# Kernel tuning notes

Hardware: AMD Instinct MI355X
Metric: run time of the kernel (lower is better)

The kernel has to match this reference:

```python
import jax, jax.numpy as jnp
import numpy as np

NUM_HEADS = 16
EMBED_DIM = 1024
HEAD_DIM = EMBED_DIM // NUM_HEADS


def setup_inputs() -> dict:
    key = jax.random.key(0)
    ks = jax.random.split(key, 9)
    B, S, D = 4, 2048, EMBED_DIM
    scale = 1.0 / np.sqrt(D)
    inp = {
        "x": jax.random.normal(ks[0], (B, S, D), dtype=jnp.float32),
        "Wq": jax.random.normal(ks[1], (D, D), dtype=jnp.float32) * scale,
        "bq": jnp.zeros((D,), dtype=jnp.float32),
        "Wk": jax.random.normal(ks[2], (D, D), dtype=jnp.float32) * scale,
        "bk": jnp.zeros((D,), dtype=jnp.float32),
        "Wv": jax.random.normal(ks[3], (D, D), dtype=jnp.float32) * scale,
        "bv": jnp.zeros((D,), dtype=jnp.float32),
        "Wo": jax.random.normal(ks[4], (D, D), dtype=jnp.float32) * scale,
        "bo": jnp.zeros((D,), dtype=jnp.float32),
    }
    return inp


def reference(x, Wq, bq, Wk, bk, Wv, bv, Wo, bo):
    # x: [B, S, D]; weights stored torch-style as [out, in] -> use x @ W.T + b
    B, S, D = x.shape
    H, Hd = NUM_HEADS, HEAD_DIM

    def proj(W, b):
        return (jnp.einsum('bsd,ed->bse', x, W) + b).reshape(B, S, H, Hd).transpose(0, 2, 1, 3)

    Q = proj(Wq, bq)  # [B, H, S, Hd]
    K = proj(Wk, bk)
    V = proj(Wv, bv)

    scores = jnp.einsum('bhqd,bhkd->bhqk', Q, K) / jnp.sqrt(jnp.float32(Hd))
    attn = jax.nn.softmax(scores, axis=-1)  # dropout is identity in eval mode
    context = jnp.einsum('bhqk,bhkd->bhqd', attn, V)
    context = context.transpose(0, 2, 1, 3).reshape(B, S, D)
    out = jnp.einsum('bsd,ed->bse', context, Wo) + bo
    return out
```

## Files before the change

### kernel.cpp

```cpp
#include <hip/hip_runtime.h>


#define LOG2E 1.4426950408889634f
#define QSCALE (0.125f * LOG2E)

typedef __bf16 bf16x8 __attribute__((ext_vector_type(8)));
typedef float f32x4 __attribute__((ext_vector_type(4)));
typedef float f32x2 __attribute__((ext_vector_type(2)));
typedef unsigned short u16x4 __attribute__((ext_vector_type(4)));
typedef unsigned short u16x8 __attribute__((ext_vector_type(8)));
typedef unsigned int u32x4 __attribute__((ext_vector_type(4)));

__device__ __forceinline__ unsigned short f2bf(float f) {
  unsigned int u = __builtin_bit_cast(unsigned int, f);
  u += 0x7fffu + ((u >> 16) & 1u);
  return (unsigned short)(u >> 16);
}

__device__ __forceinline__ unsigned int cvtpk(float a, float b) {
  unsigned int r;
  asm("v_cvt_pk_bf16_f32 %0, %1, %2" : "=v"(r) : "v"(a), "v"(b));
  return r;
}

typedef const __attribute__((address_space(1))) void* gptr_t;
typedef __attribute__((address_space(3))) void* lptr_t;
__device__ __forceinline__ void gload16(const void* g, void* l) {
  __builtin_amdgcn_global_load_lds((gptr_t)g, (lptr_t)l, 16, 0, 0);
}

__global__ __launch_bounds__(256) void k_cvt(const float* __restrict__ x,
                                             const float* __restrict__ Wq, const float* __restrict__ Wk,
                                             const float* __restrict__ Wv, const float* __restrict__ Wo,
                                             unsigned short* __restrict__ xb, unsigned short* __restrict__ Wb) {
  int gi = (blockIdx.x * 256 + threadIdx.x) * 4;
  if (gi < 8388608) {
    f32x4 v = *(const f32x4*)(x + gi);
    u16x4 o; o[0] = f2bf(v[0]); o[1] = f2bf(v[1]); o[2] = f2bf(v[2]); o[3] = f2bf(v[3]);
    *(u16x4*)(xb + gi) = o;
  } else {
    int i = gi - 8388608;
    int wsel = i >> 20;
    int loc = i & 1048575;
    const float* src = (wsel == 0) ? Wq : (wsel == 1) ? Wk : (wsel == 2) ? Wv : Wo;
    float sc = (wsel == 0) ? QSCALE : 1.0f;
    f32x4 v = *(const f32x4*)(src + loc);
    u16x4 o; o[0] = f2bf(v[0] * sc); o[1] = f2bf(v[1] * sc); o[2] = f2bf(v[2] * sc); o[3] = f2bf(v[3] * sc);
    *(u16x4*)(Wb + i) = o;
  }
}

__global__ __launch_bounds__(256, 3) void k_gemm_qkv(
    const unsigned short* __restrict__ xb, const unsigned short* __restrict__ Wb,
    const float* __restrict__ bq, const float* __restrict__ bk, const float* __restrict__ bv,
    unsigned short* __restrict__ Qb, unsigned short* __restrict__ Kb, unsigned short* __restrict__ Vtb) {
  __shared__ unsigned short As[2 * 4096];
  __shared__ unsigned short Bs[2 * 4096];
  const int tid = threadIdx.x;
  const int lane = tid & 63;
  const int w = tid >> 6;
  const int wm = w & 1;
  const int wn = w >> 1;
  const int lin = blockIdx.x + (blockIdx.y << 3) + (blockIdx.z << 9);
  const int swz = (lin & 7) * 192 + (lin >> 3);
  const int z = swz >> 9;
  const int m0 = ((swz >> 3) & 63) << 7;
  const int n0 = (swz & 7) << 7;
  const unsigned short* W = Wb + ((size_t)z << 20);

  const int sR = tid >> 3;
  const int sc_ = (tid & 7) ^ (sR & 7);
  const int mrow0 = 2 * sR + (sc_ >> 2);
  const int kc0 = (sc_ & 3) << 3;
  const unsigned short* srcA = xb + (size_t)(m0 + mrow0) * 1024 + kc0;
  const unsigned short* srcB = W + (size_t)(n0 + mrow0) * 1024 + kc0;
  unsigned short* dstA = As + tid * 8;
  unsigned short* dstB = Bs + tid * 8;

  const int fr = lane & 15;
  const int kq = lane >> 4;
  int aoff[4], boff[4];
#pragma unroll
  for (int t = 0; t < 4; ++t) {
    int ra = wm * 64 + t * 16 + fr;
    aoff[t] = ((ra >> 1) << 6) + (((((ra & 1) << 2) + kq) ^ ((ra >> 1) & 7)) << 3);
    int rb = wn * 64 + t * 16 + fr;
    boff[t] = ((rb >> 1) << 6) + (((((rb & 1) << 2) + kq) ^ ((rb >> 1) & 7)) << 3);
  }

  f32x4 zero4 = {0.f, 0.f, 0.f, 0.f};
  f32x4 acc[4][4];
#pragma unroll
  for (int i = 0; i < 4; ++i)
#pragma unroll
    for (int jj = 0; jj < 4; ++jj) acc[i][jj] = zero4;

  gload16(srcA, dstA);
  gload16(srcA + 65536, dstA + 2048);
  gload16(srcB, dstB);
  gload16(srcB + 65536, dstB + 2048);

  int cur = 0;
  for (int kt = 0; kt < 32; ++kt) {
    const int kon = ((kt + 1) & 31) << 5;
    const int soff = (cur ^ 1) << 12;
    gload16(srcA + kon, dstA + soff);
    gload16(srcA + 65536 + kon, dstA + soff + 2048);
    gload16(srcB + kon, dstB + soff);
    gload16(srcB + 65536 + kon, dstB + soff + 2048);

    asm volatile("s_waitcnt vmcnt(4)" ::: "memory");
    __builtin_amdgcn_s_barrier();

    const unsigned short* Ac = As + (cur << 12);
    const unsigned short* Bc = Bs + (cur << 12);
    bf16x8 af[4], bfr[4];
#pragma unroll
    for (int mt = 0; mt < 4; ++mt) af[mt] = *(const bf16x8*)&Ac[aoff[mt]];
#pragma unroll
    for (int nt = 0; nt < 4; ++nt) bfr[nt] = *(const bf16x8*)&Bc[boff[nt]];

    asm volatile("s_waitcnt lgkmcnt(0)" ::: "memory");
    __builtin_amdgcn_s_barrier();

    __builtin_amdgcn_s_setprio(1);
#pragma unroll
    for (int mt = 0; mt < 4; ++mt)
#pragma unroll
      for (int nt = 0; nt < 4; ++nt)
        acc[mt][nt] = __builtin_amdgcn_mfma_f32_16x16x32_bf16(af[mt], bfr[nt], acc[mt][nt], 0, 0, 0);
    __builtin_amdgcn_s_setprio(0);
    cur ^= 1;
  }

  const float* bias = (z == 0) ? bq : (z == 1) ? bk : bv;
  const float bsc = (z == 0) ? QSCALE : 1.0f;
  const int rg = kq << 2;
#pragma unroll
  for (int mt = 0; mt < 4; ++mt) {
    const int mb = m0 + wm * 64 + mt * 16 + rg;
    const int b = mb >> 11;
    const int s = mb & 2047;
#pragma unroll
    for (int nt = 0; nt < 4; ++nt) {
      const int n = n0 + wn * 64 + nt * 16 + fr;
      const float bvv = bias[n] * bsc;
      const int h = n >> 6;
      const int d = n & 63;
      if (z == 2) {
        u16x4 pk;
#pragma unroll
        for (int r = 0; r < 4; ++r) pk[r] = f2bf(acc[mt][nt][r] + bvv);
        const int pbase = (s & ~31) | ((s & 12) << 1) | ((s & 16) >> 2);
        *(u16x4*)&Vtb[(((size_t)(b * 16 + h) << 6) + d) * 2048 + pbase] = pk;
      } else {
        unsigned short* O = (z == 0) ? Qb : Kb;
#pragma unroll
        for (int r = 0; r < 4; ++r)
          O[(((size_t)(b * 16 + h) << 11) + s + r) * 64 + d] = f2bf(acc[mt][nt][r] + bvv);
      }
    }
  }
}

__global__ __launch_bounds__(512, 4) void k_flash(
    const unsigned short* __restrict__ Qb, const unsigned short* __restrict__ Kb,
    const unsigned short* __restrict__ Vtb, unsigned short* __restrict__ Ctx) {
  __shared__ unsigned short Ks[2 * 128 * 64];
  __shared__ unsigned short Vts[64 * 128];
  const int tid = threadIdx.x;
  const int lane = tid & 63;
  const int wq = tid >> 6;
  const int fr = lane & 15;
  const int qd = lane >> 4;
  const int lin = blockIdx.x + (blockIdx.y << 3);
  const int swz = ((lin & 7) << 6) + (lin >> 3);
  const int bh = swz >> 3;
  const int q0 = (swz & 7) << 8;
  const size_t hoff = (size_t)bh << 17;
  const unsigned short* Qh = Qb + hoff + ((size_t)q0 << 6);

  const unsigned short* kg[2];
  const unsigned short* vg[2];
  unsigned short* kl[2];
  unsigned short* vl[2];
#pragma unroll
  for (int p = 0; p < 2; ++p) {
    int slot = p * 512 + tid;
    int kr = slot >> 3, ch = slot & 7;
    kg[p] = Kb + hoff + (size_t)kr * 64 + ((ch ^ (kr & 7)) << 3);
    kl[p] = Ks + slot * 8;
    int dr = slot >> 4, ch2 = slot & 15;
    vg[p] = Vtb + hoff + (size_t)dr * 2048 + ((ch2 ^ (dr & 15)) << 3);
    vl[p] = Vts + slot * 8;
  }

  int kbase[2];
#pragma unroll
  for (int ds = 0; ds < 2; ++ds)
    kbase[ds] = fr * 64 + (((ds * 4 + qd) ^ (fr & 7)) << 3);
  int vbase[4];
#pragma unroll
  for (int ks = 0; ks < 4; ++ks)
    vbase[ks] = fr * 128 + (((ks * 4 + qd) ^ fr) << 3);

  bf16x8 qf[2][2];
#pragma unroll
  for (int qt = 0; qt < 2; ++qt)
#pragma unroll
    for (int ds = 0; ds < 2; ++ds)
      qf[qt][ds] = *(const bf16x8*)&Qh[(wq * 32 + qt * 16 + fr) * 64 + ds * 32 + qd * 8];

  f32x4 zero4 = {0.f, 0.f, 0.f, 0.f};
  f32x4 o_acc[2][4];
  f32x2 l2[2] = {{0.f, 0.f}, {0.f, 0.f}};
#pragma unroll
  for (int mt = 0; mt < 2; ++mt)
#pragma unroll
    for (int dt = 0; dt < 4; ++dt) o_acc[mt][dt] = zero4;

#pragma unroll
  for (int p = 0; p < 2; ++p) gload16(kg[p], kl[p]);
#pragma unroll
  for (int p = 0; p < 2; ++p) kg[p] += 128 * 64;
  __syncthreads();

  int curoff = 0;
  for (int j = 0; j < 16; ++j) {
#pragma unroll
    for (int p = 0; p < 2; ++p) gload16(vg[p], vl[p]);
#pragma unroll
    for (int p = 0; p < 2; ++p) gload16(kg[p], kl[p] + (curoff ^ 8192));
#pragma unroll
    for (int p = 0; p < 2; ++p) { kg[p] += 128 * 64; vg[p] += 128; }

    const unsigned short* Kc = Ks + curoff;
    u32x4 pfw[2][4];
#pragma unroll
    for (int ks = 0; ks < 4; ++ks) {
      f32x4 st0[2], st1[2];
      st0[0] = zero4; st0[1] = zero4; st1[0] = zero4; st1[1] = zero4;
      __builtin_amdgcn_s_setprio(1);
#pragma unroll
      for (int ds = 0; ds < 2; ++ds) {
        bf16x8 kf0 = *(const bf16x8*)&Kc[kbase[ds] + (2 * ks) * 1024];
        bf16x8 kf1 = *(const bf16x8*)&Kc[kbase[ds] + (2 * ks + 1) * 1024];
        st0[0] = __builtin_amdgcn_mfma_f32_16x16x32_bf16(kf0, qf[0][ds], st0[0], 0, 0, 0);
        st0[1] = __builtin_amdgcn_mfma_f32_16x16x32_bf16(kf0, qf[1][ds], st0[1], 0, 0, 0);
        st1[0] = __builtin_amdgcn_mfma_f32_16x16x32_bf16(kf1, qf[0][ds], st1[0], 0, 0, 0);
        st1[1] = __builtin_amdgcn_mfma_f32_16x16x32_bf16(kf1, qf[1][ds], st1[1], 0, 0, 0);
      }
      __builtin_amdgcn_s_setprio(0);
#pragma unroll
      for (int mt = 0; mt < 2; ++mt) {
#pragma unroll
        for (int r = 0; r < 4; ++r) {
          st0[mt][r] = __builtin_amdgcn_exp2f(st0[mt][r]);
          st1[mt][r] = __builtin_amdgcn_exp2f(st1[mt][r]);
        }
        f32x2 s01 = {st0[mt][0], st0[mt][1]};
        f32x2 s23 = {st0[mt][2], st0[mt][3]};
        f32x2 t01 = {st1[mt][0], st1[mt][1]};
        f32x2 t23 = {st1[mt][2], st1[mt][3]};
        l2[mt] += (s01 + s23) + (t01 + t23);
        u32x4 pk;
        pk[0] = cvtpk(st0[mt][0], st0[mt][1]);
        pk[1] = cvtpk(st0[mt][2], st0[mt][3]);
        pk[2] = cvtpk(st1[mt][0], st1[mt][1]);
        pk[3] = cvtpk(st1[mt][2], st1[mt][3]);
        pfw[mt][ks] = pk;
      }
    }

    asm volatile("s_waitcnt vmcnt(2)" ::: "memory");
    __builtin_amdgcn_s_barrier();

    __builtin_amdgcn_s_setprio(1);
#pragma unroll
    for (int ks = 0; ks < 4; ++ks) {
      bf16x8 pf0 = __builtin_bit_cast(bf16x8, pfw[0][ks]);
      bf16x8 pf1 = __builtin_bit_cast(bf16x8, pfw[1][ks]);
#pragma unroll
      for (int dt = 0; dt < 4; ++dt) {
        bf16x8 vf = *(const bf16x8*)&Vts[vbase[ks] + dt * 2048];
        o_acc[0][dt] = __builtin_amdgcn_mfma_f32_16x16x32_bf16(pf0, vf, o_acc[0][dt], 0, 0, 0);
        o_acc[1][dt] = __builtin_amdgcn_mfma_f32_16x16x32_bf16(pf1, vf, o_acc[1][dt], 0, 0, 0);
      }
    }
    __builtin_amdgcn_s_setprio(0);

    asm volatile("s_waitcnt vmcnt(0)" ::: "memory");
    __builtin_amdgcn_s_barrier();
    curoff ^= 8192;
  }

  float l_red[2];
#pragma unroll
  for (int mt = 0; mt < 2; ++mt) {
    float lv = l2[mt][0] + l2[mt][1];
    lv += __shfl_xor(lv, 16);
    lv += __shfl_xor(lv, 32);
    l_red[mt] = lv;
  }

  const int b = bh >> 4;
  const int h = bh & 15;
#pragma unroll
  for (int mt = 0; mt < 2; ++mt) {
#pragma unroll
    for (int r = 0; r < 4; ++r) {
      float lv = __shfl(l_red[mt], qd * 4 + r);
      float rl = 1.0f / lv;
      int s = q0 + wq * 32 + mt * 16 + qd * 4 + r;
      size_t base = (((size_t)b * 2048 + s) << 10) + (h << 6);
#pragma unroll
      for (int dt = 0; dt < 4; ++dt) Ctx[base + dt * 16 + fr] = f2bf(o_acc[mt][dt][r] * rl);
    }
  }
}

__global__ __launch_bounds__(256, 3) void k_gemm_out(
    const unsigned short* __restrict__ Ctx, const unsigned short* __restrict__ Wo,
    const float* __restrict__ bo, float* __restrict__ out) {
  __shared__ unsigned short As[2 * 4096];
  __shared__ unsigned short Bs[2 * 4096];
  const int tid = threadIdx.x;
  const int lane = tid & 63;
  const int w = tid >> 6;
  const int wm = w & 1;
  const int wn = w >> 1;
  const int lin = blockIdx.x + (blockIdx.y << 3);
  const int swz = ((lin & 7) << 6) + (lin >> 3);
  const int m0 = (swz >> 3) << 7;
  const int n0 = (swz & 7) << 7;

  const int sR = tid >> 3;
  const int sc_ = (tid & 7) ^ (sR & 7);
  const int mrow0 = 2 * sR + (sc_ >> 2);
  const int kc0 = (sc_ & 3) << 3;
  const unsigned short* srcA = Ctx + (size_t)(m0 + mrow0) * 1024 + kc0;
  const unsigned short* srcB = Wo + (size_t)(n0 + mrow0) * 1024 + kc0;
  unsigned short* dstA = As + tid * 8;
  unsigned short* dstB = Bs + tid * 8;

  const int fr = lane & 15;
  const int kq = lane >> 4;
  int aoff[4], boff[4];
#pragma unroll
  for (int t = 0; t < 4; ++t) {
    int ra = wm * 64 + t * 16 + fr;
    aoff[t] = ((ra >> 1) << 6) + (((((ra & 1) << 2) + kq) ^ ((ra >> 1) & 7)) << 3);
    int rb = wn * 64 + t * 16 + fr;
    boff[t] = ((rb >> 1) << 6) + (((((rb & 1) << 2) + kq) ^ ((rb >> 1) & 7)) << 3);
  }

  f32x4 zero4 = {0.f, 0.f, 0.f, 0.f};
  f32x4 acc[4][4];
#pragma unroll
  for (int i = 0; i < 4; ++i)
#pragma unroll
    for (int jj = 0; jj < 4; ++jj) acc[i][jj] = zero4;

  gload16(srcA, dstA);
  gload16(srcA + 65536, dstA + 2048);
  gload16(srcB, dstB);
  gload16(srcB + 65536, dstB + 2048);

  int cur = 0;
  for (int kt = 0; kt < 32; ++kt) {
    const int kon = ((kt + 1) & 31) << 5;
    const int soff = (cur ^ 1) << 12;
    gload16(srcA + kon, dstA + soff);
    gload16(srcA + 65536 + kon, dstA + soff + 2048);
    gload16(srcB + kon, dstB + soff);
    gload16(srcB + 65536 + kon, dstB + soff + 2048);

    asm volatile("s_waitcnt vmcnt(4)" ::: "memory");
    __builtin_amdgcn_s_barrier();

    const unsigned short* Ac = As + (cur << 12);
    const unsigned short* Bc = Bs + (cur << 12);
    bf16x8 af[4], bfr[4];
#pragma unroll
    for (int mt = 0; mt < 4; ++mt) af[mt] = *(const bf16x8*)&Ac[aoff[mt]];
#pragma unroll
    for (int nt = 0; nt < 4; ++nt) bfr[nt] = *(const bf16x8*)&Bc[boff[nt]];

    asm volatile("s_waitcnt lgkmcnt(0)" ::: "memory");
    __builtin_amdgcn_s_barrier();

    __builtin_amdgcn_s_setprio(1);
#pragma unroll
    for (int mt = 0; mt < 4; ++mt)
#pragma unroll
      for (int nt = 0; nt < 4; ++nt)
        acc[mt][nt] = __builtin_amdgcn_mfma_f32_16x16x32_bf16(af[mt], bfr[nt], acc[mt][nt], 0, 0, 0);
    __builtin_amdgcn_s_setprio(0);
    cur ^= 1;
  }

  const int rg = kq << 2;
#pragma unroll
  for (int mt = 0; mt < 4; ++mt) {
    const int mb = m0 + wm * 64 + mt * 16 + rg;
#pragma unroll
    for (int nt = 0; nt < 4; ++nt) {
      const int n = n0 + wn * 64 + nt * 16 + fr;
      const float bvv = bo[n];
#pragma unroll
      for (int r = 0; r < 4; ++r)
        out[(size_t)(mb + r) * 1024 + n] = acc[mt][nt][r] + bvv;
    }
  }
}

extern "C" void kernel_launch(void* const* d_in, const int* in_sizes, int n_in,
                              void* d_out, int out_size, void* d_ws, size_t ws_size,
                              hipStream_t stream) {
  (void)in_sizes; (void)n_in; (void)out_size; (void)ws_size;
  const float* x = (const float*)d_in[0];
  const float* Wq = (const float*)d_in[1];
  const float* bq = (const float*)d_in[2];
  const float* Wk = (const float*)d_in[3];
  const float* bk = (const float*)d_in[4];
  const float* Wv = (const float*)d_in[5];
  const float* bv = (const float*)d_in[6];
  const float* Wo = (const float*)d_in[7];
  const float* bo = (const float*)d_in[8];
  float* out = (float*)d_out;

  unsigned short* xb = (unsigned short*)d_ws;
  unsigned short* Wb = xb + 8388608;
  unsigned short* Qb = Wb + 4194304;
  unsigned short* Kb = Qb + 8388608;
  unsigned short* Vtb = Kb + 8388608;
  unsigned short* Ctx = xb;

  k_cvt<<<12288, 256, 0, stream>>>(x, Wq, Wk, Wv, Wo, xb, Wb);
  k_gemm_qkv<<<dim3(8, 64, 3), 256, 0, stream>>>(xb, Wb, bq, bk, bv, Qb, Kb, Vtb);
  k_flash<<<dim3(8, 64), 512, 0, stream>>>(Qb, Kb, Vtb, Ctx);
  k_gemm_out<<<dim3(8, 64), 256, 0, stream>>>(Ctx, Wb + 3 * 1048576, bo, out);
}
```

Before: 263.0 us.

## Enlarge QKV GEMM tiles to 256x256 with 512 threads and deeper K steps

Rewrites the QKV projection GEMM to use 256x256 output tiles per block with 8 waves, a K step of 64, and a new LDS layout with XOR swizzle. Inside each K step it double-buffers the A fragment reads from shared memory so they overlap the MFMAs. The grid becomes 384 blocks with a new swizzle mapping. The aim is to raise arithmetic intensity and cut global and LDS traffic per FLOP, at the cost of 128 KB of LDS, more registers per thread, and fewer blocks (384 over 256 CUs), which risks poor occupancy and tail imbalance.

```diff
diff --git a/kernel.cpp b/kernel.cpp
--- a/kernel.cpp
+++ b/kernel.cpp
@@ -50,95 +50,116 @@
   }
 }
 
-__global__ __launch_bounds__(256, 3) void k_gemm_qkv(
+__global__ __launch_bounds__(512, 2) void k_gemm_qkv(
     const unsigned short* __restrict__ xb, const unsigned short* __restrict__ Wb,
     const float* __restrict__ bq, const float* __restrict__ bk, const float* __restrict__ bv,
     unsigned short* __restrict__ Qb, unsigned short* __restrict__ Kb, unsigned short* __restrict__ Vtb) {
-  __shared__ unsigned short As[2 * 4096];
-  __shared__ unsigned short Bs[2 * 4096];
+  __shared__ unsigned short As[2 * 16384];
+  __shared__ unsigned short Bs[2 * 16384];
   const int tid = threadIdx.x;
   const int lane = tid & 63;
   const int w = tid >> 6;
-  const int wm = w & 1;
-  const int wn = w >> 1;
-  const int lin = blockIdx.x + (blockIdx.y << 3) + (blockIdx.z << 9);
-  const int swz = (lin & 7) * 192 + (lin >> 3);
-  const int z = swz >> 9;
-  const int m0 = ((swz >> 3) & 63) << 7;
-  const int n0 = (swz & 7) << 7;
+  const int wm = w >> 2;
+  const int wn = w & 3;
+  const int lin = blockIdx.x;
+  const int swz = (lin & 7) * 48 + (lin >> 3);
+  const int z = swz >> 7;
+  const int t7 = swz & 127;
+  const int m0 = (t7 >> 2) << 8;
+  const int n0 = (t7 & 3) << 8;
   const unsigned short* W = Wb + ((size_t)z << 20);
 
-  const int sR = tid >> 3;
-  const int sc_ = (tid & 7) ^ (sR & 7);
-  const int mrow0 = 2 * sR + (sc_ >> 2);
-  const int kc0 = (sc_ & 3) << 3;
-  const unsigned short* srcA = xb + (size_t)(m0 + mrow0) * 1024 + kc0;
-  const unsigned short* srcB = W + (size_t)(n0 + mrow0) * 1024 + kc0;
-  unsigned short* dstA = As + tid * 8;
-  unsigned short* dstB = Bs + tid * 8;
+  const int srow = tid >> 3;
+  const int sc_ = (tid & 7) ^ (srow & 7);
+  const unsigned short* pA = xb + (size_t)(m0 + srow) * 1024 + sc_ * 8;
+  const unsigned short* pB = W + (size_t)(n0 + srow) * 1024 + sc_ * 8;
+  unsigned short* dA = As + tid * 8;
+  unsigned short* dB = Bs + tid * 8;
 
   const int fr = lane & 15;
   const int kq = lane >> 4;
-  int aoff[4], boff[4];
-#pragma unroll
-  for (int t = 0; t < 4; ++t) {
-    int ra = wm * 64 + t * 16 + fr;
-    aoff[t] = ((ra >> 1) << 6) + (((((ra & 1) << 2) + kq) ^ ((ra >> 1) & 7)) << 3);
-    int rb = wn * 64 + t * 16 + fr;
-    boff[t] = ((rb >> 1) << 6) + (((((rb & 1) << 2) + kq) ^ ((rb >> 1) & 7)) << 3);
+  int aoff[2], boff[2];
+#pragma unroll
+  for (int ds = 0; ds < 2; ++ds) {
+    const int ps = ((ds * 4 + kq) ^ (fr & 7)) << 3;
+    aoff[ds] = (wm * 128 + fr) * 64 + ps;
+    boff[ds] = (wn * 64 + fr) * 64 + ps;
   }
 
   f32x4 zero4 = {0.f, 0.f, 0.f, 0.f};
-  f32x4 acc[4][4];
-#pragma unroll
-  for (int i = 0; i < 4; ++i)
+  f32x4 acc[8][4];
+#pragma unroll
+  for (int i = 0; i < 8; ++i)
 #pragma unroll
     for (int jj = 0; jj < 4; ++jj) acc[i][jj] = zero4;
 
-  gload16(srcA, dstA);
-  gload16(srcA + 65536, dstA + 2048);
-  gload16(srcB, dstB);
-  gload16(srcB + 65536, dstB + 2048);
-
-  int cur = 0;
-  for (int kt = 0; kt < 32; ++kt) {
-    const int kon = ((kt + 1) & 31) << 5;
-    const int soff = (cur ^ 1) << 12;
-    gload16(srcA + kon, dstA + soff);
-    gload16(srcA + 65536 + kon, dstA + soff + 2048);
-    gload16(srcB + kon, dstB + soff);
-    gload16(srcB + 65536 + kon, dstB + soff + 2048);
-
-    asm volatile("s_waitcnt vmcnt(4)" ::: "memory");
+#pragma unroll
+  for (int p = 0; p < 4; ++p) gload16(pA + p * 65536, dA + p * 4096);
+#pragma unroll
+  for (int p = 0; p < 4; ++p) gload16(pB + p * 65536, dB + p * 4096);
+  pA += 64; pB += 64;
+  __syncthreads();
+
+  for (int kt = 0; kt < 16; ++kt) {
+    const int bo = (kt & 1) << 14;
+    const int so = bo ^ 16384;
+#pragma unroll
+    for (int p = 0; p < 4; ++p) gload16(pA + p * 65536, dA + so + p * 4096);
+#pragma unroll
+    for (int p = 0; p < 4; ++p) gload16(pB + p * 65536, dB + so + p * 4096);
+    pA += 64; pB += 64;
+
+    bf16x8 bfr[8];
+#pragma unroll
+    for (int nt = 0; nt < 4; ++nt)
+#pragma unroll
+      for (int ds = 0; ds < 2; ++ds)
+        bfr[nt * 2 + ds] = *(const bf16x8*)&Bs[bo + boff[ds] + nt * 1024];
+    bf16x8 af[2][4];
+#pragma unroll
+    for (int i = 0; i < 2; ++i)
+#pragma unroll
+      for (int ds = 0; ds < 2; ++ds)
+        af[0][i * 2 + ds] = *(const bf16x8*)&As[bo + aoff[ds] + i * 1024];
+    asm volatile("s_waitcnt lgkmcnt(0)" ::: "memory");
+    __builtin_amdgcn_sched_barrier(0);
+
+#pragma unroll
+    for (int q = 0; q < 4; ++q) {
+      if (q < 3) {
+#pragma unroll
+        for (int i = 0; i < 2; ++i)
+#pragma unroll
+          for (int ds = 0; ds < 2; ++ds)
+            af[(q + 1) & 1][i * 2 + ds] =
+                *(const bf16x8*)&As[bo + aoff[ds] + (q + 1) * 2048 + i * 1024];
+      }
+      __builtin_amdgcn_s_setprio(1);
+#pragma unroll
+      for (int ds = 0; ds < 2; ++ds)
+#pragma unroll
+        for (int i = 0; i < 2; ++i)
+#pragma unroll
+          for (int nt = 0; nt < 4; ++nt)
+            acc[q * 2 + i][nt] = __builtin_amdgcn_mfma_f32_16x16x32_bf16(
+                af[q & 1][i * 2 + ds], bfr[nt * 2 + ds], acc[q * 2 + i][nt], 0, 0, 0);
+      __builtin_amdgcn_s_setprio(0);
+      if (q < 3) {
+        asm volatile("s_waitcnt lgkmcnt(0)" ::: "memory");
+        __builtin_amdgcn_sched_barrier(0);
+      }
+    }
+
+    asm volatile("s_waitcnt vmcnt(0)" ::: "memory");
     __builtin_amdgcn_s_barrier();
-
-    const unsigned short* Ac = As + (cur << 12);
-    const unsigned short* Bc = Bs + (cur << 12);
-    bf16x8 af[4], bfr[4];
-#pragma unroll
-    for (int mt = 0; mt < 4; ++mt) af[mt] = *(const bf16x8*)&Ac[aoff[mt]];
-#pragma unroll
-    for (int nt = 0; nt < 4; ++nt) bfr[nt] = *(const bf16x8*)&Bc[boff[nt]];
-
-    asm volatile("s_waitcnt lgkmcnt(0)" ::: "memory");
-    __builtin_amdgcn_s_barrier();
-
-    __builtin_amdgcn_s_setprio(1);
-#pragma unroll
-    for (int mt = 0; mt < 4; ++mt)
-#pragma unroll
-      for (int nt = 0; nt < 4; ++nt)
-        acc[mt][nt] = __builtin_amdgcn_mfma_f32_16x16x32_bf16(af[mt], bfr[nt], acc[mt][nt], 0, 0, 0);
-    __builtin_amdgcn_s_setprio(0);
-    cur ^= 1;
   }
 
   const float* bias = (z == 0) ? bq : (z == 1) ? bk : bv;
   const float bsc = (z == 0) ? QSCALE : 1.0f;
   const int rg = kq << 2;
 #pragma unroll
-  for (int mt = 0; mt < 4; ++mt) {
-    const int mb = m0 + wm * 64 + mt * 16 + rg;
+  for (int mt = 0; mt < 8; ++mt) {
+    const int mb = m0 + wm * 128 + mt * 16 + rg;
     const int b = mb >> 11;
     const int s = mb & 2047;
 #pragma unroll
@@ -437,7 +458,7 @@
   unsigned short* Ctx = xb;
 
   k_cvt<<<12288, 256, 0, stream>>>(x, Wq, Wk, Wv, Wo, xb, Wb);
-  k_gemm_qkv<<<dim3(8, 64, 3), 256, 0, stream>>>(xb, Wb, bq, bk, bv, Qb, Kb, Vtb);
+  k_gemm_qkv<<<384, 512, 0, stream>>>(xb, Wb, bq, bk, bv, Qb, Kb, Vtb);
   k_flash<<<dim3(8, 64), 512, 0, stream>>>(Qb, Kb, Vtb, Ctx);
   k_gemm_out<<<dim3(8, 64), 256, 0, stream>>>(Ctx, Wb + 3 * 1048576, bo, out);
 }
```

Measured after the change: 271.2 us. 3.1% more time.

## Double-buffer V tile alongside K to prefetch a full iteration ahead

Applied to the files above, without the earlier changes.

Doubles the V shared-memory buffer so K and V tiles for the next key block are both prefetched one iteration ahead. Each iteration now has one barrier plus a wait-then-barrier at the top, replacing the mid-iteration and end-of-iteration barriers. This hides V load latency behind the QK^T and softmax work. The cost is 16 KB more LDS per block, which may lower occupancy under the launch bounds. The last iteration wraps around and issues a redundant load of tile 0.

```diff
diff --git a/kernel.cpp b/kernel.cpp
--- a/kernel.cpp
+++ b/kernel.cpp
@@ -167,7 +167,7 @@
     const unsigned short* __restrict__ Qb, const unsigned short* __restrict__ Kb,
     const unsigned short* __restrict__ Vtb, unsigned short* __restrict__ Ctx) {
   __shared__ unsigned short Ks[2 * 128 * 64];
-  __shared__ unsigned short Vts[64 * 128];
+  __shared__ unsigned short Vts[2 * 64 * 128];
   const int tid = threadIdx.x;
   const int lane = tid & 63;
   const int wq = tid >> 6;
@@ -219,22 +219,25 @@
 #pragma unroll
     for (int dt = 0; dt < 4; ++dt) o_acc[mt][dt] = zero4;
 
-#pragma unroll
-  for (int p = 0; p < 2; ++p) gload16(kg[p], kl[p]);
-#pragma unroll
-  for (int p = 0; p < 2; ++p) kg[p] += 128 * 64;
-  __syncthreads();
-
-  int curoff = 0;
+  gload16(kg[0], kl[0]);
+  gload16(kg[1], kl[1]);
+  gload16(vg[0], vl[0]);
+  gload16(vg[1], vl[1]);
+
   for (int j = 0; j < 16; ++j) {
-#pragma unroll
-    for (int p = 0; p < 2; ++p) gload16(vg[p], vl[p]);
-#pragma unroll
-    for (int p = 0; p < 2; ++p) gload16(kg[p], kl[p] + (curoff ^ 8192));
-#pragma unroll
-    for (int p = 0; p < 2; ++p) { kg[p] += 128 * 64; vg[p] += 128; }
-
-    const unsigned short* Kc = Ks + curoff;
+    __builtin_amdgcn_s_barrier();
+    const int jn = (j + 1) & 15;
+    const int sb = ((j + 1) & 1) << 13;
+    gload16(kg[0] + jn * 8192, kl[0] + sb);
+    gload16(kg[1] + jn * 8192, kl[1] + sb);
+    gload16(vg[0] + jn * 128, vl[0] + sb);
+    gload16(vg[1] + jn * 128, vl[1] + sb);
+    asm volatile("s_waitcnt vmcnt(4)" ::: "memory");
+    __builtin_amdgcn_s_barrier();
+
+    const int cb = (j & 1) << 13;
+    const unsigned short* Kc = Ks + cb;
+
     u32x4 pfw[2][4];
 #pragma unroll
     for (int ks = 0; ks < 4; ++ks) {
@@ -272,9 +275,6 @@
       }
     }
 
-    asm volatile("s_waitcnt vmcnt(2)" ::: "memory");
-    __builtin_amdgcn_s_barrier();
-
     __builtin_amdgcn_s_setprio(1);
 #pragma unroll
     for (int ks = 0; ks < 4; ++ks) {
@@ -282,16 +282,12 @@
       bf16x8 pf1 = __builtin_bit_cast(bf16x8, pfw[1][ks]);
 #pragma unroll
       for (int dt = 0; dt < 4; ++dt) {
-        bf16x8 vf = *(const bf16x8*)&Vts[vbase[ks] + dt * 2048];
+        bf16x8 vf = *(const bf16x8*)&Vts[cb + vbase[ks] + dt * 2048];
         o_acc[0][dt] = __builtin_amdgcn_mfma_f32_16x16x32_bf16(pf0, vf, o_acc[0][dt], 0, 0, 0);
         o_acc[1][dt] = __builtin_amdgcn_mfma_f32_16x16x32_bf16(pf1, vf, o_acc[1][dt], 0, 0, 0);
       }
     }
     __builtin_amdgcn_s_setprio(0);
-
-    asm volatile("s_waitcnt vmcnt(0)" ::: "memory");
-    __builtin_amdgcn_s_barrier();
-    curoff ^= 8192;
   }
 
   float l_red[2];
```

Result: no change. 261.1 us (-0.7%).
